# Optimization experiments

Measured on AMD Instinct MI355X. Metric: run time of the kernel, lower is better.

Reference implementation:

```python
import jax, jax.numpy as jnp
import numpy as np

BN_EPS = 1e-3  # Keras BatchNormalization default epsilon

def setup_inputs() -> dict:
    key = jax.random.key(0)
    ks = jax.random.split(key, 6)
    B, H, W, C = 8, 128, 128, 128
    s = 0.05  # small init scale for weights
    return {
        "x1": jax.random.normal(ks[0], (B, H, W, C), jnp.float32),
        "x2": jax.random.normal(ks[1], (B, H, W, C), jnp.float32),
        "Wq": jax.random.normal(ks[2], (C, C), jnp.float32) * s,
        "Wk": jax.random.normal(ks[3], (C, C), jnp.float32) * s,
        "Wv": jax.random.normal(ks[4], (C, C), jnp.float32) * s,
        "Ws": jax.random.normal(ks[5], (C, C), jnp.float32) * s,
        "bs": jnp.zeros((C,), jnp.float32),
        "scale": jnp.ones((1,), jnp.float32),   # layers.Attention use_scale=True, init 1
        "gamma": jnp.ones((C,), jnp.float32),
        "beta": jnp.zeros((C,), jnp.float32),
        "mu": jnp.zeros((C,), jnp.float32),
        "var": jnp.ones((C,), jnp.float32),
    }


def reference(x1, x2, Wq, Wk, Wv, Ws, bs, scale, gamma, beta, mu, var):
    # x1, x2: [B,H,W,C].  1x1 convs with relu == per-pixel channel matmul.
    q = jax.nn.relu(jnp.einsum('bhwc,cd->bhwd', x1, Wq))  # [B,H,W,C]
    k = jax.nn.relu(jnp.einsum('bhwc,cd->bhwd', x1, Wk))
    v = jax.nn.relu(jnp.einsum('bhwc,cd->bhwd', x2, Wv))
    # After transpose [0,3,1,2], Keras Attention batches over (B,C):
    # seq axis = H (rows), feature dim = W (cols). Fold the transposes into einsum.
    scores = scale[0] * jnp.einsum('bhwc,bgwc->bchg', q, k)  # [B,C,H,H]
    attn = jax.nn.softmax(scores, axis=-1)
    # attn @ v over row axis g, then implicit transpose back to NHWC.
    o = jnp.einsum('bchg,bgwc->bhwc', attn, v)  # [B,H,W,C]
    # sigmoid 1x1 conv (with bias), then inference-mode BatchNorm.
    g = jax.nn.sigmoid(jnp.einsum('bhwc,cd->bhwd', o, Ws) + bs)
    g = gamma * (g - mu) * jax.lax.rsqrt(var + BN_EPS) + beta
    # gated residual
    return x1 + x2 * g
```

## Files before the change

kernel.cpp:

```cpp
#include <hip/hip_runtime.h>

typedef unsigned int u32;
typedef unsigned short u16;
typedef u16 u16x4 __attribute__((ext_vector_type(4)));
typedef u16 u16x8 __attribute__((ext_vector_type(8)));
typedef __bf16 bf16x8 __attribute__((ext_vector_type(8)));
typedef float f32x4 __attribute__((ext_vector_type(4)));

#define LDK 136
#define MFMA(a, b, c) __builtin_amdgcn_mfma_f32_16x16x32_bf16(a, b, c, 0, 0, 0)

__device__ __forceinline__ u16 f2b(float f) {
  u32 u = __builtin_bit_cast(u32, f);
  u = (u + 0x7fffu + ((u >> 16) & 1u)) >> 16;
  return (u16)u;
}
__device__ __forceinline__ float b2f(u16 h) {
  u32 u = ((u32)h) << 16;
  return __builtin_bit_cast(float, u);
}

__global__ void wprep(const float* __restrict__ Wq, const float* __restrict__ Wk,
                      const float* __restrict__ Wv, const float* __restrict__ Ws,
                      u16* __restrict__ wT) {
  const float* srcs[4] = {Wq, Wk, Wv, Ws};
  const float* s = srcs[blockIdx.x];
  u16* d = wT + (size_t)blockIdx.x * 16384;
  for (int idx = threadIdx.x; idx < 16384; idx += 256) {
    int i = idx >> 7, j = idx & 127;
    d[j * 128 + i] = f2b(s[idx]);
  }
}

__global__ __launch_bounds__(256, 4)
void qkv_kernel(const float* __restrict__ x1, const float* __restrict__ x2,
                const u16* __restrict__ wT,
                u16* __restrict__ q_t, u16* __restrict__ k_t, u16* __restrict__ v_t) {
  __shared__ u16 Xs[128 * LDK];

  const int t = threadIdx.x;
  const int bh = blockIdx.x;
  const int m = blockIdx.y;
  const int b = bh >> 7, h = bh & 127;
  const size_t pixbase = (size_t)bh * 16384;
  const size_t obase = (size_t)b * 2097152 + (size_t)h * 128;

  const float* xin = (m == 2) ? x2 : x1;
  u16* dst = (m == 0) ? q_t : (m == 1) ? k_t : v_t;

  const int lane = t & 63, wave = t >> 6;
  const int lrow = lane & 15, lq = lane >> 4;
  const int nstrip = wave * 32;

  const u16* wb = wT + (size_t)m * 16384;
  bf16x8 w0[4], w1[4];
#pragma unroll
  for (int kk = 0; kk < 4; ++kk) {
    int ko = kk * 32 + lq * 8;
    w0[kk] = *(const bf16x8*)&wb[(nstrip + lrow) * 128 + ko];
    w1[kk] = *(const bf16x8*)&wb[(nstrip + 16 + lrow) * 128 + ko];
  }

#pragma unroll
  for (int j = 0; j < 8; ++j) {
    int lin = j * 256 + t;
    int w = lin >> 4, c0 = (lin & 15) << 3;
    f32x4 a0 = *(const f32x4*)&xin[pixbase + lin * 8];
    f32x4 a1 = *(const f32x4*)&xin[pixbase + lin * 8 + 4];
    u16x8 p;
#pragma unroll
    for (int i = 0; i < 4; ++i) { p[i] = f2b(a0[i]); p[4 + i] = f2b(a1[i]); }
    *(u16x8*)&Xs[w * LDK + c0] = p;
  }
  __syncthreads();

  f32x4 acc[8][2];
#pragma unroll
  for (int mt = 0; mt < 8; ++mt) {
    acc[mt][0] = (f32x4){0.f, 0.f, 0.f, 0.f};
    acc[mt][1] = (f32x4){0.f, 0.f, 0.f, 0.f};
  }
#pragma unroll
  for (int kk = 0; kk < 4; ++kk) {
    int ko = kk * 32 + lq * 8;
#pragma unroll
    for (int mt = 0; mt < 8; ++mt) {
      bf16x8 a = *(const bf16x8*)&Xs[(mt * 16 + lrow) * LDK + ko];
      acc[mt][0] = MFMA(a, w0[kk], acc[mt][0]);
      acc[mt][1] = MFMA(a, w1[kk], acc[mt][1]);
    }
  }
  __syncthreads();

#pragma unroll
  for (int mt = 0; mt < 8; ++mt) {
    int w0i = mt * 16 + lq * 4;
#pragma unroll
    for (int nt = 0; nt < 2; ++nt) {
      int c = nstrip + nt * 16 + lrow;
      u16x4 p;
#pragma unroll
      for (int r = 0; r < 4; ++r) p[r] = f2b(fmaxf(acc[mt][nt][r], 0.f));
      *(u16x4*)&Xs[c * LDK + w0i] = p;
    }
  }
  __syncthreads();

#pragma unroll
  for (int j = 0; j < 8; ++j) {
    int c = j * 16 + (t >> 4), wv = (t & 15) * 8;
    *(u16x8*)&dst[obase + (size_t)c * 16384 + wv] = *(const u16x8*)&Xs[c * LDK + wv];
  }
}

__global__ __launch_bounds__(256, 2)
void attn_kernel(u16* __restrict__ q_t, const u16* __restrict__ k_t,
                 const u16* __restrict__ v_t, const float* __restrict__ scale_p) {
  __shared__ u16 Ks[128 * LDK];
  __shared__ u16 Ps[128 * LDK];

  const int t = threadIdx.x;
  const size_t base = (size_t)blockIdx.x * 16384;

  const int lane = t & 63, wave = t >> 6;
  const int lrow = lane & 15, lq = lane >> 4;
  const int hstrip = wave * 32;
  const float scl = scale_p[0];

  bf16x8 q0[4], q1[4];
#pragma unroll
  for (int kk = 0; kk < 4; ++kk) {
    int ko = kk * 32 + lq * 8;
    q0[kk] = *(const bf16x8*)&q_t[base + (hstrip + lrow) * 128 + ko];
    q1[kk] = *(const bf16x8*)&q_t[base + (hstrip + 16 + lrow) * 128 + ko];
  }
  const int g0 = (t & 15) * 8, w0v = (t >> 4) * 8;
  u16x8 vv[8];
#pragma unroll
  for (int i = 0; i < 8; ++i)
    vv[i] = *(const u16x8*)&v_t[base + (g0 + i) * 128 + w0v];
#pragma unroll
  for (int j = 0; j < 8; ++j) {
    int lin = j * 256 + t;
    int r = lin >> 4, c0 = (lin & 15) << 3;
    *(u16x8*)&Ks[r * LDK + c0] = *(const u16x8*)&k_t[base + lin * 8];
  }
  __syncthreads();

  f32x4 acc[8][2];
#pragma unroll
  for (int mt = 0; mt < 8; ++mt) {
    acc[mt][0] = (f32x4){0.f, 0.f, 0.f, 0.f};
    acc[mt][1] = (f32x4){0.f, 0.f, 0.f, 0.f};
  }
#pragma unroll
  for (int kk = 0; kk < 4; ++kk) {
    int ko = kk * 32 + lq * 8;
#pragma unroll
    for (int mt = 0; mt < 8; ++mt) {
      bf16x8 a = *(const bf16x8*)&Ks[(mt * 16 + lrow) * LDK + ko];
      acc[mt][0] = MFMA(a, q0[kk], acc[mt][0]);
      acc[mt][1] = MFMA(a, q1[kk], acc[mt][1]);
    }
  }

  float inv[2];
#pragma unroll
  for (int nt = 0; nt < 2; ++nt) {
    float mx = -1e30f;
#pragma unroll
    for (int mt = 0; mt < 8; ++mt)
#pragma unroll
      for (int r = 0; r < 4; ++r) {
        acc[mt][nt][r] *= scl;
        mx = fmaxf(mx, acc[mt][nt][r]);
      }
    mx = fmaxf(mx, __shfl_xor(mx, 16));
    mx = fmaxf(mx, __shfl_xor(mx, 32));
    float s = 0.f;
#pragma unroll
    for (int mt = 0; mt < 8; ++mt)
#pragma unroll
      for (int r = 0; r < 4; ++r) {
        float e = __expf(acc[mt][nt][r] - mx);
        acc[mt][nt][r] = e;
        s += e;
      }
    s += __shfl_xor(s, 16);
    s += __shfl_xor(s, 32);
    inv[nt] = 1.f / s;
  }
  __syncthreads();

#pragma unroll
  for (int j = 0; j < 8; ++j) {
    u16x8 tv;
#pragma unroll
    for (int i = 0; i < 8; ++i) tv[i] = vv[i][j];
    *(u16x8*)&Ks[(w0v + j) * LDK + g0] = tv;
  }
#pragma unroll
  for (int mt = 0; mt < 8; ++mt) {
    int gg0 = mt * 16 + lq * 4;
#pragma unroll
    for (int nt = 0; nt < 2; ++nt) {
      int hh = hstrip + nt * 16 + lrow;
      u16x4 p;
#pragma unroll
      for (int r = 0; r < 4; ++r) p[r] = f2b(acc[mt][nt][r] * inv[nt]);
      *(u16x4*)&Ps[hh * LDK + gg0] = p;
    }
  }
  __syncthreads();

#pragma unroll
  for (int kk = 0; kk < 4; ++kk) {
    int ko = kk * 32 + lq * 8;
    bf16x8 b0 = *(const bf16x8*)&Ps[(hstrip + lrow) * LDK + ko];
    bf16x8 b1 = *(const bf16x8*)&Ps[(hstrip + 16 + lrow) * LDK + ko];
    if (kk == 0) {
#pragma unroll
      for (int mt = 0; mt < 8; ++mt) {
        acc[mt][0] = (f32x4){0.f, 0.f, 0.f, 0.f};
        acc[mt][1] = (f32x4){0.f, 0.f, 0.f, 0.f};
      }
    }
#pragma unroll
    for (int mt = 0; mt < 8; ++mt) {
      bf16x8 a = *(const bf16x8*)&Ks[(mt * 16 + lrow) * LDK + ko];
      acc[mt][0] = MFMA(a, b0, acc[mt][0]);
      acc[mt][1] = MFMA(a, b1, acc[mt][1]);
    }
  }
  __syncthreads();

#pragma unroll
  for (int mt = 0; mt < 8; ++mt) {
    int w0i = mt * 16 + lq * 4;
#pragma unroll
    for (int nt = 0; nt < 2; ++nt) {
      int hh = hstrip + nt * 16 + lrow;
      u16x4 p;
#pragma unroll
      for (int r = 0; r < 4; ++r) p[r] = f2b(acc[mt][nt][r]);
      *(u16x4*)&Ks[hh * LDK + w0i] = p;
    }
  }
  __syncthreads();
#pragma unroll
  for (int j = 0; j < 8; ++j) {
    int hh = j * 16 + (t >> 4), wv = (t & 15) * 8;
    *(u16x8*)&q_t[base + hh * 128 + wv] = *(const u16x8*)&Ks[hh * LDK + wv];
  }
}

__global__ __launch_bounds__(256, 4)
void final_kernel(const u16* __restrict__ o_t, const u16* __restrict__ wsT,
                  const float* __restrict__ x1, const float* __restrict__ x2,
                  const float* __restrict__ bs, const float* __restrict__ gamma,
                  const float* __restrict__ beta, const float* __restrict__ mu,
                  const float* __restrict__ var, float* __restrict__ out) {
  __shared__ u16 Os[128 * LDK];
  __shared__ float bnA[128], bnB[128], bsf[128];

  const int t = threadIdx.x;
  const int bh = blockIdx.x;
  const int b = bh >> 7, h = bh & 127;
  const size_t obase = (size_t)b * 2097152 + (size_t)h * 128;
  const size_t pixbase = (size_t)bh * 16384;

  if (t < 128) {
    float a = gamma[t] * rsqrtf(var[t] + 1e-3f);
    bnA[t] = a;
    bnB[t] = beta[t] - mu[t] * a;
    bsf[t] = bs[t];
  }
  {
    int c0 = (t & 15) * 8, w0 = (t >> 4) * 8;
    u16 ov[8][8];
#pragma unroll
    for (int i = 0; i < 8; ++i)
      *(u16x8*)&ov[i][0] = *(const u16x8*)&o_t[obase + (size_t)(c0 + i) * 16384 + w0];
#pragma unroll
    for (int j = 0; j < 8; ++j) {
      u16x8 tv;
#pragma unroll
      for (int i = 0; i < 8; ++i) tv[i] = ov[i][j];
      *(u16x8*)&Os[(w0 + j) * LDK + c0] = tv;
    }
  }
  __syncthreads();

  const int lane = t & 63, wave = t >> 6;
  const int lrow = lane & 15, lq = lane >> 4;
  const int wstrip = wave * 32;

  f32x4 acc[8][2];
#pragma unroll
  for (int mt = 0; mt < 8; ++mt) {
    acc[mt][0] = (f32x4){0.f, 0.f, 0.f, 0.f};
    acc[mt][1] = (f32x4){0.f, 0.f, 0.f, 0.f};
  }
#pragma unroll
  for (int kk = 0; kk < 4; ++kk) {
    int ko = kk * 32 + lq * 8;
    bf16x8 b0 = *(const bf16x8*)&Os[(wstrip + lrow) * LDK + ko];
    bf16x8 b1 = *(const bf16x8*)&Os[(wstrip + 16 + lrow) * LDK + ko];
#pragma unroll
    for (int mt = 0; mt < 8; ++mt) {
      bf16x8 a = *(const bf16x8*)&wsT[(mt * 16 + lrow) * 128 + ko];
      acc[mt][0] = MFMA(a, b0, acc[mt][0]);
      acc[mt][1] = MFMA(a, b1, acc[mt][1]);
    }
  }

#pragma unroll
  for (int mt = 0; mt < 8; ++mt) {
    int d0 = mt * 16 + lq * 4;
    f32x4 A4 = *(const f32x4*)&bnA[d0];
    f32x4 B4 = *(const f32x4*)&bnB[d0];
    f32x4 S4 = *(const f32x4*)&bsf[d0];
#pragma unroll
    for (int nt = 0; nt < 2; ++nt) {
      int w = wstrip + nt * 16 + lrow;
      size_t off = pixbase + (size_t)w * 128 + d0;
      f32x4 a1v = *(const f32x4*)&x1[off];
      f32x4 a2v = *(const f32x4*)&x2[off];
      f32x4 r;
#pragma unroll
      for (int r4 = 0; r4 < 4; ++r4) {
        float sv = acc[mt][nt][r4] + S4[r4];
        float sg = 1.f / (1.f + __expf(-sv));
        float g = A4[r4] * sg + B4[r4];
        r[r4] = a1v[r4] + a2v[r4] * g;
      }
      *(f32x4*)&out[off] = r;
    }
  }
}

extern "C" void kernel_launch(void* const* d_in, const int* in_sizes, int n_in,
                              void* d_out, int out_size, void* d_ws, size_t ws_size,
                              hipStream_t stream) {
  const float* x1 = (const float*)d_in[0];
  const float* x2 = (const float*)d_in[1];
  const float* Wq = (const float*)d_in[2];
  const float* Wk = (const float*)d_in[3];
  const float* Wv = (const float*)d_in[4];
  const float* Ws = (const float*)d_in[5];
  const float* bs = (const float*)d_in[6];
  const float* scale = (const float*)d_in[7];
  const float* gamma = (const float*)d_in[8];
  const float* beta = (const float*)d_in[9];
  const float* mu = (const float*)d_in[10];
  const float* var = (const float*)d_in[11];
  float* outp = (float*)d_out;

  u16* q_t = (u16*)d_ws;
  u16* k_t = q_t + 16777216;
  u16* v_t = k_t + 16777216;
  u16* wT = v_t + 16777216;

  wprep<<<dim3(4), dim3(256), 0, stream>>>(Wq, Wk, Wv, Ws, wT);
  qkv_kernel<<<dim3(1024, 3), dim3(256), 0, stream>>>(x1, x2, wT, q_t, k_t, v_t);
  attn_kernel<<<dim3(1024), dim3(256), 0, stream>>>(q_t, k_t, v_t, scale);
  final_kernel<<<dim3(1024), dim3(256), 0, stream>>>(q_t, wT + 3 * 16384, x1, x2, bs,
                                                     gamma, beta, mu, var, outp);
}
```

Measured before the change: 320.8 us.

## Swizzle LDS tiles, shuffle softmax probs in registers, raise attn occupancy

Applies an XOR swizzle to every shared-memory tile index to cut LDS bank conflicts on the transposed writes and MFMA operand reads. In the attention kernel the probability matrix no longer goes through a second LDS buffer. Instead it is packed to bf16 pairs and redistributed into MFMA B-operand layout with cross-lane shuffles, which halves LDS use and allows launch_bounds to rise from 2 to 3 blocks. The V load is moved after QK^T to overlap with the MFMAs and lower register pressure, and output packing uses 32-bit pairs. The cost is extra shuffle instructions and a risk of register spills at the higher occupancy target.

```diff
diff --git a/kernel.cpp b/kernel.cpp
--- a/kernel.cpp
+++ b/kernel.cpp
@@ -4,10 +4,13 @@
 typedef unsigned short u16;
 typedef u16 u16x4 __attribute__((ext_vector_type(4)));
 typedef u16 u16x8 __attribute__((ext_vector_type(8)));
+typedef u32 u32x2 __attribute__((ext_vector_type(2)));
+typedef u32 u32x4 __attribute__((ext_vector_type(4)));
 typedef __bf16 bf16x8 __attribute__((ext_vector_type(8)));
 typedef float f32x4 __attribute__((ext_vector_type(4)));
 
 #define LDK 136
+#define TIDX(r, c) ((r) * LDK + ((c) ^ (((r) & 3) << 5)))
 #define MFMA(a, b, c) __builtin_amdgcn_mfma_f32_16x16x32_bf16(a, b, c, 0, 0, 0)
 
 __device__ __forceinline__ u16 f2b(float f) {
@@ -18,6 +21,9 @@
 __device__ __forceinline__ float b2f(u16 h) {
   u32 u = ((u32)h) << 16;
   return __builtin_bit_cast(float, u);
+}
+__device__ __forceinline__ u32 pk2(float lo, float hi) {
+  return (u32)f2b(lo) | ((u32)f2b(hi) << 16);
 }
 
 __global__ void wprep(const float* __restrict__ Wq, const float* __restrict__ Wk,
@@ -70,7 +76,7 @@
     u16x8 p;
 #pragma unroll
     for (int i = 0; i < 4; ++i) { p[i] = f2b(a0[i]); p[4 + i] = f2b(a1[i]); }
-    *(u16x8*)&Xs[w * LDK + c0] = p;
+    *(u16x8*)&Xs[TIDX(w, c0)] = p;
   }
   __syncthreads();
 
@@ -85,7 +91,7 @@
     int ko = kk * 32 + lq * 8;
 #pragma unroll
     for (int mt = 0; mt < 8; ++mt) {
-      bf16x8 a = *(const bf16x8*)&Xs[(mt * 16 + lrow) * LDK + ko];
+      bf16x8 a = *(const bf16x8*)&Xs[TIDX(mt * 16 + lrow, ko)];
       acc[mt][0] = MFMA(a, w0[kk], acc[mt][0]);
       acc[mt][1] = MFMA(a, w1[kk], acc[mt][1]);
     }
@@ -98,10 +104,10 @@
 #pragma unroll
     for (int nt = 0; nt < 2; ++nt) {
       int c = nstrip + nt * 16 + lrow;
-      u16x4 p;
-#pragma unroll
-      for (int r = 0; r < 4; ++r) p[r] = f2b(fmaxf(acc[mt][nt][r], 0.f));
-      *(u16x4*)&Xs[c * LDK + w0i] = p;
+      u32x2 p;
+      p[0] = pk2(fmaxf(acc[mt][nt][0], 0.f), fmaxf(acc[mt][nt][1], 0.f));
+      p[1] = pk2(fmaxf(acc[mt][nt][2], 0.f), fmaxf(acc[mt][nt][3], 0.f));
+      *(u32x2*)&Xs[TIDX(c, w0i)] = p;
     }
   }
   __syncthreads();
@@ -109,15 +115,14 @@
 #pragma unroll
   for (int j = 0; j < 8; ++j) {
     int c = j * 16 + (t >> 4), wv = (t & 15) * 8;
-    *(u16x8*)&dst[obase + (size_t)c * 16384 + wv] = *(const u16x8*)&Xs[c * LDK + wv];
-  }
-}
-
-__global__ __launch_bounds__(256, 2)
+    *(u16x8*)&dst[obase + (size_t)c * 16384 + wv] = *(const u16x8*)&Xs[TIDX(c, wv)];
+  }
+}
+
+__global__ __launch_bounds__(256, 3)
 void attn_kernel(u16* __restrict__ q_t, const u16* __restrict__ k_t,
                  const u16* __restrict__ v_t, const float* __restrict__ scale_p) {
   __shared__ u16 Ks[128 * LDK];
-  __shared__ u16 Ps[128 * LDK];
 
   const int t = threadIdx.x;
   const size_t base = (size_t)blockIdx.x * 16384;
@@ -134,16 +139,11 @@
     q0[kk] = *(const bf16x8*)&q_t[base + (hstrip + lrow) * 128 + ko];
     q1[kk] = *(const bf16x8*)&q_t[base + (hstrip + 16 + lrow) * 128 + ko];
   }
-  const int g0 = (t & 15) * 8, w0v = (t >> 4) * 8;
-  u16x8 vv[8];
-#pragma unroll
-  for (int i = 0; i < 8; ++i)
-    vv[i] = *(const u16x8*)&v_t[base + (g0 + i) * 128 + w0v];
 #pragma unroll
   for (int j = 0; j < 8; ++j) {
     int lin = j * 256 + t;
     int r = lin >> 4, c0 = (lin & 15) << 3;
-    *(u16x8*)&Ks[r * LDK + c0] = *(const u16x8*)&k_t[base + lin * 8];
+    *(u16x8*)&Ks[TIDX(r, c0)] = *(const u16x8*)&k_t[base + lin * 8];
   }
   __syncthreads();
 
@@ -158,11 +158,17 @@
     int ko = kk * 32 + lq * 8;
 #pragma unroll
     for (int mt = 0; mt < 8; ++mt) {
-      bf16x8 a = *(const bf16x8*)&Ks[(mt * 16 + lrow) * LDK + ko];
+      bf16x8 a = *(const bf16x8*)&Ks[TIDX(mt * 16 + lrow, ko)];
       acc[mt][0] = MFMA(a, q0[kk], acc[mt][0]);
       acc[mt][1] = MFMA(a, q1[kk], acc[mt][1]);
     }
   }
+
+  const int w0v = (t & 15) * 8, g0 = (t >> 4) * 8;
+  u16x8 vv[8];
+#pragma unroll
+  for (int i = 0; i < 8; ++i)
+    vv[i] = *(const u16x8*)&v_t[base + (size_t)(g0 + i) * 128 + w0v];
 
   float inv[2];
 #pragma unroll
@@ -190,6 +196,15 @@
     s += __shfl_xor(s, 32);
     inv[nt] = 1.f / s;
   }
+
+  u32 pk[8][2][2];
+#pragma unroll
+  for (int mt = 0; mt < 8; ++mt)
+#pragma unroll
+    for (int nt = 0; nt < 2; ++nt) {
+      pk[mt][nt][0] = pk2(acc[mt][nt][0] * inv[nt], acc[mt][nt][1] * inv[nt]);
+      pk[mt][nt][1] = pk2(acc[mt][nt][2] * inv[nt], acc[mt][nt][3] * inv[nt]);
+    }
   __syncthreads();
 
 #pragma unroll
@@ -197,27 +212,32 @@
     u16x8 tv;
 #pragma unroll
     for (int i = 0; i < 8; ++i) tv[i] = vv[i][j];
-    *(u16x8*)&Ks[(w0v + j) * LDK + g0] = tv;
-  }
-#pragma unroll
-  for (int mt = 0; mt < 8; ++mt) {
-    int gg0 = mt * 16 + lq * 4;
-#pragma unroll
-    for (int nt = 0; nt < 2; ++nt) {
-      int hh = hstrip + nt * 16 + lrow;
-      u16x4 p;
-#pragma unroll
-      for (int r = 0; r < 4; ++r) p[r] = f2b(acc[mt][nt][r] * inv[nt]);
-      *(u16x4*)&Ps[hh * LDK + gg0] = p;
-    }
-  }
-  __syncthreads();
-
-#pragma unroll
-  for (int kk = 0; kk < 4; ++kk) {
-    int ko = kk * 32 + lq * 8;
-    bf16x8 b0 = *(const bf16x8*)&Ps[(hstrip + lrow) * LDK + ko];
-    bf16x8 b1 = *(const bf16x8*)&Ps[(hstrip + 16 + lrow) * LDK + ko];
+    *(u16x8*)&Ks[TIDX(w0v + j, g0)] = tv;
+  }
+  __syncthreads();
+
+  const int s01 = lrow + 32 * (lq & 1);
+  const int s23 = s01 + 16;
+  const bool hi = (lq & 2);
+#pragma unroll
+  for (int kk = 0; kk < 4; ++kk) {
+    int ko = kk * 32 + lq * 8;
+    u32x4 bd[2];
+#pragma unroll
+    for (int nt = 0; nt < 2; ++nt) {
+      u32 a0 = pk[2 * kk][nt][0], a1 = pk[2 * kk][nt][1];
+      u32 c0 = pk[2 * kk + 1][nt][0], c1 = pk[2 * kk + 1][nt][1];
+      u32 l0 = (u32)__shfl((int)a0, s01), h0 = (u32)__shfl((int)c0, s01);
+      u32 l1 = (u32)__shfl((int)a1, s01), h1 = (u32)__shfl((int)c1, s01);
+      u32 l2 = (u32)__shfl((int)a0, s23), h2 = (u32)__shfl((int)c0, s23);
+      u32 l3 = (u32)__shfl((int)a1, s23), h3 = (u32)__shfl((int)c1, s23);
+      bd[nt][0] = hi ? h0 : l0;
+      bd[nt][1] = hi ? h1 : l1;
+      bd[nt][2] = hi ? h2 : l2;
+      bd[nt][3] = hi ? h3 : l3;
+    }
+    bf16x8 bb0 = __builtin_bit_cast(bf16x8, bd[0]);
+    bf16x8 bb1 = __builtin_bit_cast(bf16x8, bd[1]);
     if (kk == 0) {
 #pragma unroll
       for (int mt = 0; mt < 8; ++mt) {
@@ -227,9 +247,9 @@
     }
 #pragma unroll
     for (int mt = 0; mt < 8; ++mt) {
-      bf16x8 a = *(const bf16x8*)&Ks[(mt * 16 + lrow) * LDK + ko];
-      acc[mt][0] = MFMA(a, b0, acc[mt][0]);
-      acc[mt][1] = MFMA(a, b1, acc[mt][1]);
+      bf16x8 a = *(const bf16x8*)&Ks[TIDX(mt * 16 + lrow, ko)];
+      acc[mt][0] = MFMA(a, bb0, acc[mt][0]);
+      acc[mt][1] = MFMA(a, bb1, acc[mt][1]);
     }
   }
   __syncthreads();
@@ -240,17 +260,17 @@
 #pragma unroll
     for (int nt = 0; nt < 2; ++nt) {
       int hh = hstrip + nt * 16 + lrow;
-      u16x4 p;
-#pragma unroll
-      for (int r = 0; r < 4; ++r) p[r] = f2b(acc[mt][nt][r]);
-      *(u16x4*)&Ks[hh * LDK + w0i] = p;
+      u32x2 p;
+      p[0] = pk2(acc[mt][nt][0], acc[mt][nt][1]);
+      p[1] = pk2(acc[mt][nt][2], acc[mt][nt][3]);
+      *(u32x2*)&Ks[TIDX(hh, w0i)] = p;
     }
   }
   __syncthreads();
 #pragma unroll
   for (int j = 0; j < 8; ++j) {
     int hh = j * 16 + (t >> 4), wv = (t & 15) * 8;
-    *(u16x8*)&q_t[base + hh * 128 + wv] = *(const u16x8*)&Ks[hh * LDK + wv];
+    *(u16x8*)&q_t[base + hh * 128 + wv] = *(const u16x8*)&Ks[TIDX(hh, wv)];
   }
 }
 
@@ -276,17 +296,17 @@
     bsf[t] = bs[t];
   }
   {
-    int c0 = (t & 15) * 8, w0 = (t >> 4) * 8;
+    int cb = (t >> 4) * 8, w0 = (t & 15) * 8;
     u16 ov[8][8];
 #pragma unroll
     for (int i = 0; i < 8; ++i)
-      *(u16x8*)&ov[i][0] = *(const u16x8*)&o_t[obase + (size_t)(c0 + i) * 16384 + w0];
+      *(u16x8*)&ov[i][0] = *(const u16x8*)&o_t[obase + (size_t)(cb + i) * 16384 + w0];
 #pragma unroll
     for (int j = 0; j < 8; ++j) {
       u16x8 tv;
 #pragma unroll
       for (int i = 0; i < 8; ++i) tv[i] = ov[i][j];
-      *(u16x8*)&Os[(w0 + j) * LDK + c0] = tv;
+      *(u16x8*)&Os[TIDX(w0 + j, cb)] = tv;
     }
   }
   __syncthreads();
@@ -304,8 +324,8 @@
 #pragma unroll
   for (int kk = 0; kk < 4; ++kk) {
     int ko = kk * 32 + lq * 8;
-    bf16x8 b0 = *(const bf16x8*)&Os[(wstrip + lrow) * LDK + ko];
-    bf16x8 b1 = *(const bf16x8*)&Os[(wstrip + 16 + lrow) * LDK + ko];
+    bf16x8 b0 = *(const bf16x8*)&Os[TIDX(wstrip + lrow, ko)];
+    bf16x8 b1 = *(const bf16x8*)&Os[TIDX(wstrip + 16 + lrow, ko)];
 #pragma unroll
     for (int mt = 0; mt < 8; ++mt) {
       bf16x8 a = *(const bf16x8*)&wsT[(mt * 16 + lrow) * 128 + ko];
```

New measurement: 329.3 us. 1.03x slower.
